# Kernel optimization log

Measured on AMD Instinct MI355X. Metric: run time of the kernel, lower is better.

## Reference

```python
import jax, jax.numpy as jnp
import numpy as np

E = 25_600_000
N = 100_000

def setup_inputs() -> dict:
    key = jax.random.key(0)
    k1, k2, k3 = jax.random.split(key, 3)
    edge_weight = jax.random.uniform(k1, (E,), dtype=jnp.float32, minval=1e-3, maxval=1.0)
    src = jax.random.randint(k2, (E,), 0, N, dtype=jnp.int32)
    dst = jax.random.randint(k3, (E,), 0, N, dtype=jnp.int32)
    return {"edge_weight": edge_weight, "src": src, "dst": dst, "num_nodes": N}

def reference(edge_weight, src, dst, num_nodes):
    eps = 0.0
    # norm='both': out-degree weighted sum over src (reversed-graph scatter),
    # in-degree weighted sum over dst, then per-edge gather-multiply.
    out_deg = jax.ops.segment_sum(edge_weight, src, num_segments=num_nodes)  # [N]
    in_deg = jax.ops.segment_sum(edge_weight, dst, num_segments=num_nodes)   # [N]
    src_norm = jax.lax.rsqrt(out_deg + eps)  # pow(deg, -0.5)
    dst_norm = jax.lax.rsqrt(in_deg + eps)
    return src_norm[src] * dst_norm[dst] * edge_weight  # [E]
```

## Files before the change

kernel.cpp:

```cpp
#include <hip/hip_runtime.h>

#define TPB 256

typedef float ntf4 __attribute__((ext_vector_type(4)));
typedef int   nti4 __attribute__((ext_vector_type(4)));

#define SCAT_TPB 1024
#define S_RANGE  20352
#define SCAT_HALF_GRID 510
#define SCAT_GRID 1020

__device__ __forceinline__ unsigned xcc_id() {
    unsigned v;
    asm volatile("s_getreg_b32 %0, hwreg(HW_REG_XCC_ID)" : "=s"(v));
    return v & 7u;
}

__device__ __forceinline__ int calc_R(unsigned long long ws_bytes, int N) {
    unsigned long long ws_floats = ws_bytes / 4ull;
    unsigned long long r = ws_floats / (unsigned long long)(2 * N);
    if (r > 8ull) r = 8ull;
    if (r < 1ull) r = 1ull;
    return (int)r;
}

__global__ void ewn_zero_kernel(float* __restrict__ ws,
                                const int* __restrict__ pN,
                                unsigned long long ws_bytes) {
    int N = *pN;
    int R = calc_R(ws_bytes, N);
    long long total = (long long)R * 2 * N;
    for (long long i = blockIdx.x * (long long)blockDim.x + threadIdx.x; i < total;
         i += (long long)gridDim.x * blockDim.x) {
        ws[i] = 0.0f;
    }
}

__global__ __launch_bounds__(SCAT_TPB, 8) void ewn_scatter_kernel(
        const float* __restrict__ w,
        const int* __restrict__ src,
        const int* __restrict__ dst,
        float* __restrict__ ws,
        const int* __restrict__ pN,
        unsigned long long ws_bytes,
        int E) {
    __shared__ float h[S_RANGE];

    const int N = *pN;
    const int R = calc_R(ws_bytes, N);

    const int half_grid = (int)gridDim.x / 2;
    const int pass = (blockIdx.x >= half_grid) ? 1 : 0;
    const int pbid = (int)blockIdx.x - pass * half_grid;
    const int* __restrict__ idx = pass ? dst : src;

    int NR = (N + S_RANGE - 1) / S_RANGE;
    if (NR < 1) NR = 1;
    int M = half_grid / NR;
    if (M < 1) M = 1;

    if (pbid >= NR * M) return;
    const int m = pbid / NR;
    const int r = pbid % NR;
    const int lo = r * S_RANGE;

    for (int i = threadIdx.x; i < S_RANGE; i += SCAT_TPB) h[i] = 0.0f;
    __syncthreads();

    long long stripe = (((long long)E + M - 1) / M + 3ll) & ~3ll;
    long long jstart = (long long)m * stripe;
    long long jend   = jstart + stripe;
    if (jend > E) jend = E;

    const long long STEP = (long long)SCAT_TPB * 4;

    long long j0 = jstart + (long long)threadIdx.x * 4;
    for (; j0 + 3 < jend; j0 += STEP) {
        float4 wv = *(const float4*)(w + j0);
        int4   sv = *(const int4*)(idx + j0);
        int t;
        t = sv.x - lo; if ((unsigned)t < (unsigned)S_RANGE) unsafeAtomicAdd(&h[t], wv.x);
        t = sv.y - lo; if ((unsigned)t < (unsigned)S_RANGE) unsafeAtomicAdd(&h[t], wv.y);
        t = sv.z - lo; if ((unsigned)t < (unsigned)S_RANGE) unsafeAtomicAdd(&h[t], wv.z);
        t = sv.w - lo; if ((unsigned)t < (unsigned)S_RANGE) unsafeAtomicAdd(&h[t], wv.w);
    }
    if (j0 < jend) {
        for (long long j = j0; j < jend; ++j) {
            float wj = w[j];
            int t = idx[j] - lo;
            if ((unsigned)t < (unsigned)S_RANGE) unsafeAtomicAdd(&h[t], wj);
        }
    }
    __syncthreads();

    const unsigned xcc = xcc_id();
    int hi = N - lo;
    if (hi > S_RANGE) hi = S_RANGE;

    if (R == 8) {
        float* deg = ws + (unsigned long long)xcc * 2ull * N
                        + (pass ? (unsigned long long)N : 0ull);
        for (int i = threadIdx.x; i < hi; i += SCAT_TPB) {
            __hip_atomic_fetch_add(&deg[lo + i], h[i], __ATOMIC_RELAXED, __HIP_MEMORY_SCOPE_WORKGROUP);
        }
    } else {
        float* deg = ws + (unsigned long long)(xcc % (unsigned)R) * 2ull * N
                        + (pass ? (unsigned long long)N : 0ull);
        for (int i = threadIdx.x; i < hi; i += SCAT_TPB) {
            atomicAdd(&deg[lo + i], h[i]);
        }
    }
}

__global__ void ewn_reduce_norm_kernel(float* __restrict__ ws,
                                       const int* __restrict__ pN,
                                       unsigned long long ws_bytes) {
    int N = *pN;
    int R = calc_R(ws_bytes, N);
    long long n2 = 2ll * N;
    for (long long i = blockIdx.x * (long long)blockDim.x + threadIdx.x; i < n2;
         i += (long long)gridDim.x * blockDim.x) {
        float s = 0.0f;
        for (int r = 0; r < R; ++r) s += ws[(long long)r * n2 + i];
        ws[i] = 1.0f / sqrtf(s);
    }
}

__global__ __launch_bounds__(TPB, 8) void ewn_gather_kernel(
        const float* __restrict__ w,
        const int* __restrict__ src,
        const int* __restrict__ dst,
        const float* __restrict__ ws,
        const int* __restrict__ pN,
        float* __restrict__ out,
        int E) {
    const int N = *pN;
    const float* norm_out = ws;
    const float* norm_in  = ws + N;

    const long long tid  = (long long)blockIdx.x * blockDim.x + threadIdx.x;
    const long long half = (long long)gridDim.x * blockDim.x * 4;
    long long ia = tid * 4;
    long long ib = ia + half;

    if (ib + 3 < E) {
        ntf4 wva = __builtin_nontemporal_load((const ntf4*)(w + ia));
        nti4 sva = __builtin_nontemporal_load((const nti4*)(src + ia));
        nti4 dva = __builtin_nontemporal_load((const nti4*)(dst + ia));
        ntf4 wvb = __builtin_nontemporal_load((const ntf4*)(w + ib));
        nti4 svb = __builtin_nontemporal_load((const nti4*)(src + ib));
        nti4 dvb = __builtin_nontemporal_load((const nti4*)(dst + ib));
        __builtin_amdgcn_sched_barrier(0);
        float sa0 = norm_out[sva.x], sa1 = norm_out[sva.y], sa2 = norm_out[sva.z], sa3 = norm_out[sva.w];
        float da0 = norm_in[dva.x],  da1 = norm_in[dva.y],  da2 = norm_in[dva.z],  da3 = norm_in[dva.w];
        float sb0 = norm_out[svb.x], sb1 = norm_out[svb.y], sb2 = norm_out[svb.z], sb3 = norm_out[svb.w];
        float db0 = norm_in[dvb.x],  db1 = norm_in[dvb.y],  db2 = norm_in[dvb.z],  db3 = norm_in[dvb.w];
        __builtin_amdgcn_sched_barrier(0);
        ntf4 ova, ovb;
        ova.x = sa0 * da0 * wva.x;
        ova.y = sa1 * da1 * wva.y;
        ova.z = sa2 * da2 * wva.z;
        ova.w = sa3 * da3 * wva.w;
        ovb.x = sb0 * db0 * wvb.x;
        ovb.y = sb1 * db1 * wvb.y;
        ovb.z = sb2 * db2 * wvb.z;
        ovb.w = sb3 * db3 * wvb.w;
        __builtin_nontemporal_store(ova, (ntf4*)(out + ia));
        __builtin_nontemporal_store(ovb, (ntf4*)(out + ib));
    } else {
        for (int b = 0; b < 2; ++b) {
            long long i4 = b ? ib : ia;
            if (i4 + 3 < E) {
                ntf4 wv = __builtin_nontemporal_load((const ntf4*)(w + i4));
                nti4 sv = __builtin_nontemporal_load((const nti4*)(src + i4));
                nti4 dv = __builtin_nontemporal_load((const nti4*)(dst + i4));
                ntf4 ov;
                ov.x = norm_out[sv.x] * norm_in[dv.x] * wv.x;
                ov.y = norm_out[sv.y] * norm_in[dv.y] * wv.y;
                ov.z = norm_out[sv.z] * norm_in[dv.z] * wv.z;
                ov.w = norm_out[sv.w] * norm_in[dv.w] * wv.w;
                __builtin_nontemporal_store(ov, (ntf4*)(out + i4));
            } else if (i4 < E) {
                for (long long j = i4; j < E && j < i4 + 4; ++j) {
                    out[j] = norm_out[src[j]] * norm_in[dst[j]] * w[j];
                }
            }
        }
    }
}

extern "C" void kernel_launch(void* const* d_in, const int* in_sizes, int n_in,
                              void* d_out, int out_size, void* d_ws, size_t ws_size,
                              hipStream_t stream) {
    const float* edge_weight = (const float*)d_in[0];
    const int*   src         = (const int*)d_in[1];
    const int*   dst         = (const int*)d_in[2];
    const int*   pN          = (const int*)d_in[3];
    float* out = (float*)d_out;
    const int E = in_sizes[0];
    float* ws = (float*)d_ws;
    unsigned long long wsb = (unsigned long long)ws_size;

    int nBlocksGather = (int)(((long long)E / 8 + TPB - 1) / TPB);
    if (nBlocksGather < 1) nBlocksGather = 1;

    ewn_zero_kernel<<<1024, TPB, 0, stream>>>(ws, pN, wsb);
    ewn_scatter_kernel<<<SCAT_GRID, SCAT_TPB, 0, stream>>>(edge_weight, src, dst, ws, pN, wsb, E);
    ewn_reduce_norm_kernel<<<1024, TPB, 0, stream>>>(ws, pN, wsb);
    ewn_gather_kernel<<<nBlocksGather, TPB, 0, stream>>>(edge_weight, src, dst, ws, pN, out, E);
}
```

Before: 724.6 us.

## Remap scatter blocks so same-stripe blocks share an XCC and prefetch loads

The scatter grid is reorganised so that the ten blocks (5 range slots by 2 passes) covering one edge stripe sit on the same XCC, using blockIdx modulo 8. Their repeated reads of the same w/src/dst stripe should then hit that XCC's L2 rather than going to HBM. Each block loops over node ranges r0, r0+5, and the inner loop software-prefetches the next float4/int4 before issuing the LDS atomics. The grid grows to 1040 blocks with 102 stripes. This relies on the round-robin block-to-XCC dispatch assumption and adds an extra sync per range.

```diff
diff --git a/kernel.cpp b/kernel.cpp
--- a/kernel.cpp
+++ b/kernel.cpp
@@ -7,8 +7,8 @@
 
 #define SCAT_TPB 1024
 #define S_RANGE  20352
-#define SCAT_HALF_GRID 510
-#define SCAT_GRID 1020
+#define SCAT_M   102
+#define SCAT_GRID 1040
 
 __device__ __forceinline__ unsigned xcc_id() {
     unsigned v;
@@ -48,67 +48,82 @@
 
     const int N = *pN;
     const int R = calc_R(ws_bytes, N);
-
-    const int half_grid = (int)gridDim.x / 2;
-    const int pass = (blockIdx.x >= half_grid) ? 1 : 0;
-    const int pbid = (int)blockIdx.x - pass * half_grid;
-    const int* __restrict__ idx = pass ? dst : src;
-
     int NR = (N + S_RANGE - 1) / S_RANGE;
     if (NR < 1) NR = 1;
-    int M = half_grid / NR;
-    if (M < 1) M = 1;
-
-    if (pbid >= NR * M) return;
-    const int m = pbid / NR;
-    const int r = pbid % NR;
-    const int lo = r * S_RANGE;
-
-    for (int i = threadIdx.x; i < S_RANGE; i += SCAT_TPB) h[i] = 0.0f;
-    __syncthreads();
-
-    long long stripe = (((long long)E + M - 1) / M + 3ll) & ~3ll;
+
+    const int x   = (int)blockIdx.x & 7;
+    const int k   = (int)blockIdx.x >> 3;
+    const int sub = k % 10;
+    const int gi  = k / 10;
+    const int m   = gi * 8 + x;
+    if (m >= SCAT_M) return;
+    const int pass = sub & 1;
+    const int r0   = sub >> 1;
+    const int* __restrict__ idx = pass ? dst : src;
+
+    long long stripe = (((long long)E + SCAT_M - 1) / SCAT_M + 3ll) & ~3ll;
     long long jstart = (long long)m * stripe;
     long long jend   = jstart + stripe;
     if (jend > E) jend = E;
 
     const long long STEP = (long long)SCAT_TPB * 4;
-
-    long long j0 = jstart + (long long)threadIdx.x * 4;
-    for (; j0 + 3 < jend; j0 += STEP) {
-        float4 wv = *(const float4*)(w + j0);
-        int4   sv = *(const int4*)(idx + j0);
-        int t;
-        t = sv.x - lo; if ((unsigned)t < (unsigned)S_RANGE) unsafeAtomicAdd(&h[t], wv.x);
-        t = sv.y - lo; if ((unsigned)t < (unsigned)S_RANGE) unsafeAtomicAdd(&h[t], wv.y);
-        t = sv.z - lo; if ((unsigned)t < (unsigned)S_RANGE) unsafeAtomicAdd(&h[t], wv.z);
-        t = sv.w - lo; if ((unsigned)t < (unsigned)S_RANGE) unsafeAtomicAdd(&h[t], wv.w);
-    }
-    if (j0 < jend) {
-        for (long long j = j0; j < jend; ++j) {
-            float wj = w[j];
-            int t = idx[j] - lo;
-            if ((unsigned)t < (unsigned)S_RANGE) unsafeAtomicAdd(&h[t], wj);
-        }
-    }
-    __syncthreads();
-
     const unsigned xcc = xcc_id();
-    int hi = N - lo;
-    if (hi > S_RANGE) hi = S_RANGE;
-
-    if (R == 8) {
-        float* deg = ws + (unsigned long long)xcc * 2ull * N
-                        + (pass ? (unsigned long long)N : 0ull);
-        for (int i = threadIdx.x; i < hi; i += SCAT_TPB) {
-            __hip_atomic_fetch_add(&deg[lo + i], h[i], __ATOMIC_RELAXED, __HIP_MEMORY_SCOPE_WORKGROUP);
-        }
-    } else {
-        float* deg = ws + (unsigned long long)(xcc % (unsigned)R) * 2ull * N
-                        + (pass ? (unsigned long long)N : 0ull);
-        for (int i = threadIdx.x; i < hi; i += SCAT_TPB) {
-            atomicAdd(&deg[lo + i], h[i]);
-        }
+
+    for (int r = r0; r < NR; r += 5) {
+        const int lo = r * S_RANGE;
+
+        for (int i = threadIdx.x; i < S_RANGE; i += SCAT_TPB) h[i] = 0.0f;
+        __syncthreads();
+
+        long long j0 = jstart + (long long)threadIdx.x * 4;
+        if (j0 + 3 < jend) {
+            float4 wv = *(const float4*)(w + j0);
+            int4   sv = *(const int4*)(idx + j0);
+            long long jn = j0 + STEP;
+            for (; jn + 3 < jend; jn += STEP) {
+                float4 wv2 = *(const float4*)(w + jn);
+                int4   sv2 = *(const int4*)(idx + jn);
+                int t;
+                t = sv.x - lo; if ((unsigned)t < (unsigned)S_RANGE) unsafeAtomicAdd(&h[t], wv.x);
+                t = sv.y - lo; if ((unsigned)t < (unsigned)S_RANGE) unsafeAtomicAdd(&h[t], wv.y);
+                t = sv.z - lo; if ((unsigned)t < (unsigned)S_RANGE) unsafeAtomicAdd(&h[t], wv.z);
+                t = sv.w - lo; if ((unsigned)t < (unsigned)S_RANGE) unsafeAtomicAdd(&h[t], wv.w);
+                wv = wv2; sv = sv2;
+            }
+            {
+                int t;
+                t = sv.x - lo; if ((unsigned)t < (unsigned)S_RANGE) unsafeAtomicAdd(&h[t], wv.x);
+                t = sv.y - lo; if ((unsigned)t < (unsigned)S_RANGE) unsafeAtomicAdd(&h[t], wv.y);
+                t = sv.z - lo; if ((unsigned)t < (unsigned)S_RANGE) unsafeAtomicAdd(&h[t], wv.z);
+                t = sv.w - lo; if ((unsigned)t < (unsigned)S_RANGE) unsafeAtomicAdd(&h[t], wv.w);
+            }
+            j0 = jn;
+        }
+        if (j0 < jend) {
+            for (long long j = j0; j < jend; ++j) {
+                float wj = w[j];
+                int t = idx[j] - lo;
+                if ((unsigned)t < (unsigned)S_RANGE) unsafeAtomicAdd(&h[t], wj);
+            }
+        }
+        __syncthreads();
+
+        int hi = N - lo;
+        if (hi > S_RANGE) hi = S_RANGE;
+        if (R == 8) {
+            float* deg = ws + (unsigned long long)xcc * 2ull * N
+                            + (pass ? (unsigned long long)N : 0ull);
+            for (int i = threadIdx.x; i < hi; i += SCAT_TPB) {
+                __hip_atomic_fetch_add(&deg[lo + i], h[i], __ATOMIC_RELAXED, __HIP_MEMORY_SCOPE_WORKGROUP);
+            }
+        } else {
+            float* deg = ws + (unsigned long long)(xcc % (unsigned)R) * 2ull * N
+                            + (pass ? (unsigned long long)N : 0ull);
+            for (int i = threadIdx.x; i < hi; i += SCAT_TPB) {
+                atomicAdd(&deg[lo + i], h[i]);
+            }
+        }
+        __syncthreads();
     }
 }
 
```

Measured after the change: 746.6 us. 1.03x slower.
